# Optimization experiments

Hardware: AMD Instinct MI355X
Metric: run time of the kernel (lower is better)

## Reference

```python
import jax, jax.numpy as jnp
import numpy as np

OUT_H = 7
OUT_W = 7
SPATIAL_SCALE = 0.25
SAMPLING_RATIO = 2  # exact sampling branch (sampling_ratio > 0)
ALIGNED = True


def setup_inputs() -> dict:
    key = jax.random.key(0)
    k1, k2, k3, k4 = jax.random.split(key, 4)
    feat = jax.random.normal(k1, (4, 256, 100, 100), dtype=jnp.float32)
    # rois[K,5]: (batch_idx, x1, y1, x2, y2) in image coords (image ~400px since scale=0.25)
    K = 512
    bidx = jax.random.randint(k2, (K,), 0, 4).astype(jnp.float32)
    xy1 = jax.random.uniform(k3, (K, 2), minval=0.0, maxval=300.0, dtype=jnp.float32)
    wh = jax.random.uniform(k4, (K, 2), minval=20.0, maxval=99.0, dtype=jnp.float32)
    xy2 = xy1 + wh
    rois = jnp.concatenate([bidx[:, None], xy1[:, 0:1], xy1[:, 1:2], xy2[:, 0:1], xy2[:, 1:2]], axis=1)
    return {"input": feat, "rois": rois}


def _roi_align(feat, rois):
    N, C, H, W = feat.shape
    b = rois[:, 0].astype(jnp.int32)  # [K]
    offset = 0.5 if ALIGNED else 0.0
    sw = rois[:, 1] * SPATIAL_SCALE - offset
    sh = rois[:, 2] * SPATIAL_SCALE - offset
    ew = rois[:, 3] * SPATIAL_SCALE - offset
    eh = rois[:, 4] * SPATIAL_SCALE - offset
    rw = ew - sw
    rh = eh - sh
    if not ALIGNED:
        rw = jnp.maximum(rw, 1.0)
        rh = jnp.maximum(rh, 1.0)
    bin_h = rh / OUT_H  # [K]
    bin_w = rw / OUT_W

    ph = jnp.arange(OUT_H, dtype=feat.dtype)
    pw = jnp.arange(OUT_W, dtype=feat.dtype)
    samp = jnp.arange(SAMPLING_RATIO, dtype=feat.dtype) + 0.5  # (i + 0.5)

    # y: [K, OUT_H, SR], x: [K, OUT_W, SR]
    y = sh[:, None, None] + ph[None, :, None] * bin_h[:, None, None] + samp[None, None, :] * (bin_h / SAMPLING_RATIO)[:, None, None]
    x = sw[:, None, None] + pw[None, :, None] * bin_w[:, None, None] + samp[None, None, :] * (bin_w / SAMPLING_RATIO)[:, None, None]

    # bilinear interpolation indices/weights (matches _bilinear_interpolate)
    y = jnp.maximum(y, 0.0)
    x = jnp.maximum(x, 0.0)
    yl = y.astype(jnp.int32)
    xl = x.astype(jnp.int32)
    yh = jnp.where(yl >= H - 1, H - 1, yl + 1)
    yl = jnp.where(yl >= H - 1, H - 1, yl)
    xh = jnp.where(xl >= W - 1, W - 1, xl + 1)
    xl = jnp.where(xl >= W - 1, W - 1, xl)
    ly = y - yl.astype(feat.dtype)
    lx = x - xl.astype(feat.dtype)
    hy = 1.0 - ly
    hx = 1.0 - lx

    def gather(yi, xi):
        # yi: [K,PH,IY], xi: [K,PW,IX] -> [K,PH,IY,PW,IX,C]
        return feat[b[:, None, None, None, None], :,
                    yi[:, :, :, None, None],
                    xi[:, None, None, :, :]]

    v1 = gather(yl, xl)
    v2 = gather(yl, xh)
    v3 = gather(yh, xl)
    v4 = gather(yh, xh)

    out = (jnp.einsum('kpi,kqj,kpiqjc->kcpq', hy, hx, v1)
           + jnp.einsum('kpi,kqj,kpiqjc->kcpq', hy, lx, v2)
           + jnp.einsum('kpi,kqj,kpiqjc->kcpq', ly, hx, v3)
           + jnp.einsum('kpi,kqj,kpiqjc->kcpq', ly, lx, v4))
    count = float(max(SAMPLING_RATIO * SAMPLING_RATIO, 1))
    return out / count  # [K, C, OUT_H, OUT_W]


def reference(input, rois):
    return _roi_align(input, rois)
```

## Files before the change

kernel.cpp:

```cpp
#include <hip/hip_runtime.h>


#define FEAT_C 256
#define FEAT_H 100
#define FEAT_W 100
#define HW     10000
#define NROI   512
#define NBINS  49
#define CPB    8
#define GROUPS 32
#define NPAIR  4
#define YS     14
#define RSTR   60
#define PAIRSTR (YS * RSTR)

typedef float f32x2 __attribute__((ext_vector_type(2)));

__device__ __forceinline__ void samp_geo(float s, float bsz, int idx, int sr_i,
                                         int& lo, float& fr) {
    float v = s + bsz * ((float)idx + ((float)sr_i + 0.5f) * 0.5f);
    v = fmaxf(v, 0.0f);
    int l = (int)v;
    if (l > FEAT_H - 1) l = FEAT_H - 1;
    fr = v - (float)l;
    lo = l;
}

__global__ __launch_bounds__(256, 8) void roialign_fwd(
    const float* __restrict__ feat,
    const float* __restrict__ rois,
    float* __restrict__ out)
{
    __shared__ __align__(16) float s_rows[NPAIR * PAIRSTR];
    __shared__ __align__(16) int2  s_xt[YS];

    const int bid = blockIdx.x;
    const int k   = bid >> 5;
    const int cg  = bid & (GROUPS - 1);
    const int tid = threadIdx.x;

    const float* r = rois + k * 5;
    const int   b  = (int)r[0];
    const float sw = r[1] * 0.25f - 0.5f;
    const float sh = r[2] * 0.25f - 0.5f;
    const float ew = r[3] * 0.25f - 0.5f;
    const float eh = r[4] * 0.25f - 0.5f;
    const float bh = (eh - sh) * (1.0f / 7.0f);
    const float bw = (ew - sw) * (1.0f / 7.0f);

    int x0; float fd;
    samp_geo(sw, bw, 0, 0, x0, fd);
    const int ax0 = x0 & ~3;

    if (tid < YS) {
        int lo; float fr;
        samp_geo(sw, bw, tid >> 1, tid & 1, lo, fr);
        if (lo >= FEAT_W - 1) fr = 0.0f;
        s_xt[tid] = make_int2((lo - ax0) * 2, __float_as_int(fr));
    }

    if (tid < 2 * 98) {
        const int half = tid >= 98;
        const int sid  = tid - 98 * half;
        const int ys   = (sid * 9363) >> 16;
        const int q    = sid - ys * 7;

        int yl; float fry;
        samp_geo(sh, bh, ys >> 1, ys & 1, yl, fry);
        int yh = yl + 1; if (yh > FEAT_H - 1) yh = FEAT_H - 1;
        const float hyw = 1.0f - fry, lyw = fry;

        int col = ax0 + q * 4;
        if (col > FEAT_W - 4) col = FEAT_W - 4;

        const float* fb = feat + (size_t)(b * FEAT_C + cg * CPB) * HW
                        + yl * FEAT_W + col;
        const int dyh = (yh - yl) * FEAT_W;
        float* dbase = s_rows + ys * RSTR + q * 8;

        for (int p = 2 * half; p < 2 * half + 2; p++) {
            const float* c0 = fb + (2 * p) * HW;
            const float* c1 = c0 + HW;
            float4 L0 = *(const float4*)(c0);
            float4 H0 = *(const float4*)(c0 + dyh);
            float4 L1 = *(const float4*)(c1);
            float4 H1 = *(const float4*)(c1 + dyh);
            float4 r0, r1;
            r0.x = L0.x * hyw + H0.x * lyw;  r0.y = L0.y * hyw + H0.y * lyw;
            r0.z = L0.z * hyw + H0.z * lyw;  r0.w = L0.w * hyw + H0.w * lyw;
            r1.x = L1.x * hyw + H1.x * lyw;  r1.y = L1.y * hyw + H1.y * lyw;
            r1.z = L1.z * hyw + H1.z * lyw;  r1.w = L1.w * hyw + H1.w * lyw;
            float* d = dbase + p * PAIRSTR;
            *(float4*)(d)     = make_float4(r0.x, r1.x, r0.y, r1.y);
            *(float4*)(d + 4) = make_float4(r0.z, r1.z, r0.w, r1.w);
        }
    }
    __syncthreads();

    if (tid < 4 * NBINS) {
        const int cp  = (tid * 335) >> 14;
        const int bin = tid - cp * NBINS;
        const int ph  = (bin * 37) >> 8;
        const int pw  = bin - ph * 7;

        const int4 xg = *(const int4*)(&s_xt[2 * pw]);
        const float lx0 = __int_as_float(xg.y), hx0 = 1.0f - lx0;
        const float lx1 = __int_as_float(xg.w), hx1 = 1.0f - lx1;

        const float* P = s_rows + cp * PAIRSTR + (2 * ph) * RSTR;
        f32x2 acc = {0.0f, 0.0f};
        #pragma unroll
        for (int iy = 0; iy < 2; iy++) {
            const float* row = P + iy * RSTR;
            const f32x2* A = (const f32x2*)(row + xg.x);
            f32x2 a0 = A[0], a1 = A[1];
            const f32x2* B = (const f32x2*)(row + xg.z);
            f32x2 b0 = B[0], b1 = B[1];
            acc += a0 * hx0 + a1 * lx0;
            acc += b0 * hx1 + b1 * lx1;
        }
        acc *= 0.25f;

        float* ob = out + ((size_t)k * FEAT_C + cg * CPB + cp * 2) * NBINS + bin;
        ob[0]     = acc.x;
        ob[NBINS] = acc.y;
    }
}

extern "C" void kernel_launch(void* const* d_in, const int* in_sizes, int n_in,
                              void* d_out, int out_size, void* d_ws, size_t ws_size,
                              hipStream_t stream) {
    const float* feat = (const float*)d_in[0];
    const float* rois = (const float*)d_in[1];
    float*       outp = (float*)d_out;
    roialign_fwd<<<dim3(NROI * GROUPS), dim3(256), 0, stream>>>(feat, rois, outp);
}
```

Before: 105.2 us.

## Stage ROI patches via direct global-to-LDS loads with double-buffered channel loop

Each block now handles 32 channels of one ROI instead of 8, iterating over 8 items of 4 channels. A 25x28 feature patch per channel is copied straight into LDS with global_load_lds, double-buffered so the next item's load overlaps the current item's interpolation. The y-interpolation moves from the staging step to the consumer. This cuts block count and the per-block ROI geometry setup, and avoids the register round-trip on loads. The cost is more syncs per block, lower occupancy, and a fixed 25-row patch that must cover the ROI extent.

```diff
diff --git a/kernel.cpp b/kernel.cpp
--- a/kernel.cpp
+++ b/kernel.cpp
@@ -7,14 +7,13 @@
 #define HW     10000
 #define NROI   512
 #define NBINS  49
-#define CPB    8
-#define GROUPS 32
-#define NPAIR  4
-#define YS     14
-#define RSTR   60
-#define PAIRSTR (YS * RSTR)
-
-typedef float f32x2 __attribute__((ext_vector_type(2)));
+#define CPI    4
+#define ITEMS  8
+#define PROWS  25
+#define PSTR   28
+#define CBYTES (PROWS * PSTR * 4)
+#define BUFDW  (CPI * PROWS * PSTR)
+#define BUFBYTES (BUFDW * 4)
 
 __device__ __forceinline__ void samp_geo(float s, float bsz, int idx, int sr_i,
                                          int& lo, float& fr) {
@@ -26,104 +25,109 @@
     lo = l;
 }
 
-__global__ __launch_bounds__(256, 8) void roialign_fwd(
+__global__ __launch_bounds__(256, 7) void roialign_fwd(
     const float* __restrict__ feat,
     const float* __restrict__ rois,
     float* __restrict__ out)
 {
-    __shared__ __align__(16) float s_rows[NPAIR * PAIRSTR];
-    __shared__ __align__(16) int2  s_xt[YS];
+    __shared__ __align__(16) float s_patch[2 * BUFDW];
+    __shared__ __align__(16) int2  s_yt[14];
+    __shared__ __align__(16) int2  s_xt[14];
 
-    const int bid = blockIdx.x;
-    const int k   = bid >> 5;
-    const int cg  = bid & (GROUPS - 1);
-    const int tid = threadIdx.x;
+    const int bid  = blockIdx.x;
+    const int k    = bid >> 3;
+    const int cgrp = bid & 7;
+    const int tid  = threadIdx.x;
 
     const float* r = rois + k * 5;
     const int   b  = (int)r[0];
-    const float sw = r[1] * 0.25f - 0.5f;
-    const float sh = r[2] * 0.25f - 0.5f;
-    const float ew = r[3] * 0.25f - 0.5f;
-    const float eh = r[4] * 0.25f - 0.5f;
+    const float sw = r[1] * 0.25f - 0.5f, sh = r[2] * 0.25f - 0.5f;
+    const float ew = r[3] * 0.25f - 0.5f, eh = r[4] * 0.25f - 0.5f;
     const float bh = (eh - sh) * (1.0f / 7.0f);
     const float bw = (ew - sw) * (1.0f / 7.0f);
 
-    int x0; float fd;
-    samp_geo(sw, bw, 0, 0, x0, fd);
-    const int ax0 = x0 & ~3;
+    int y0, yM, x0, xM; float fd;
+    samp_geo(sh, bh, 0, 0, y0, fd);  samp_geo(sh, bh, 6, 1, yM, fd);
+    samp_geo(sw, bw, 0, 0, x0, fd);  samp_geo(sw, bw, 6, 1, xM, fd);
+    const int ax0  = x0 & ~3;
+    const int rows = yM - y0 + 2;
 
-    if (tid < YS) {
+    if (tid < 14) {
         int lo; float fr;
-        samp_geo(sw, bw, tid >> 1, tid & 1, lo, fr);
+        samp_geo(sh, bh, tid >> 1, tid & 1, lo, fr);
+        s_yt[tid] = make_int2((lo - y0) * (PSTR * 4), __float_as_int(fr));
+    } else if (tid >= 32 && tid < 46) {
+        int t = tid - 32; int lo; float fr;
+        samp_geo(sw, bw, t >> 1, t & 1, lo, fr);
         if (lo >= FEAT_W - 1) fr = 0.0f;
-        s_xt[tid] = make_int2((lo - ax0) * 2, __float_as_int(fr));
+        s_xt[t] = make_int2((lo - ax0) * 4, __float_as_int(fr));
     }
 
-    if (tid < 2 * 98) {
-        const int half = tid >= 98;
-        const int sid  = tid - 98 * half;
-        const int ys   = (sid * 9363) >> 16;
-        const int q    = sid - ys * 7;
+    const int  spy = (tid * 9363) >> 16;
+    const int  sq  = tid - spy * 7;
+    int sy = y0 + spy; if (sy > FEAT_H - 1) sy = FEAT_H - 1;
+    int sc = ax0 + sq * 4; if (sc > FEAT_W - 4) sc = FEAT_W - 4;
+    const int  goff   = sy * FEAT_W + sc;
+    const bool stager = tid < rows * 7;
+    const int  wid    = __builtin_amdgcn_readfirstlane(tid >> 6);
+    const float* fblk = feat + (size_t)(b * FEAT_C + cgrp * 32) * HW;
 
-        int yl; float fry;
-        samp_geo(sh, bh, ys >> 1, ys & 1, yl, fry);
-        int yh = yl + 1; if (yh > FEAT_H - 1) yh = FEAT_H - 1;
-        const float hyw = 1.0f - fry, lyw = fry;
+    auto dma = [&](int item, int selb) {
+        if (stager) {
+            const float* g0 = fblk + (size_t)item * (CPI * HW) + goff;
+            char* l0 = (char*)s_patch + selb * BUFBYTES + wid * 1024;
+            #pragma unroll
+            for (int c = 0; c < CPI; c++)
+                __builtin_amdgcn_global_load_lds(
+                    (const __attribute__((address_space(1))) void*)(g0 + c * HW),
+                    (__attribute__((address_space(3))) void*)(l0 + c * CBYTES),
+                    16, 0, 0);
+        }
+    };
 
-        int col = ax0 + q * 4;
-        if (col > FEAT_W - 4) col = FEAT_W - 4;
-
-        const float* fb = feat + (size_t)(b * FEAT_C + cg * CPB) * HW
-                        + yl * FEAT_W + col;
-        const int dyh = (yh - yl) * FEAT_W;
-        float* dbase = s_rows + ys * RSTR + q * 8;
-
-        for (int p = 2 * half; p < 2 * half + 2; p++) {
-            const float* c0 = fb + (2 * p) * HW;
-            const float* c1 = c0 + HW;
-            float4 L0 = *(const float4*)(c0);
-            float4 H0 = *(const float4*)(c0 + dyh);
-            float4 L1 = *(const float4*)(c1);
-            float4 H1 = *(const float4*)(c1 + dyh);
-            float4 r0, r1;
-            r0.x = L0.x * hyw + H0.x * lyw;  r0.y = L0.y * hyw + H0.y * lyw;
-            r0.z = L0.z * hyw + H0.z * lyw;  r0.w = L0.w * hyw + H0.w * lyw;
-            r1.x = L1.x * hyw + H1.x * lyw;  r1.y = L1.y * hyw + H1.y * lyw;
-            r1.z = L1.z * hyw + H1.z * lyw;  r1.w = L1.w * hyw + H1.w * lyw;
-            float* d = dbase + p * PAIRSTR;
-            *(float4*)(d)     = make_float4(r0.x, r1.x, r0.y, r1.y);
-            *(float4*)(d + 4) = make_float4(r0.z, r1.z, r0.w, r1.w);
-        }
-    }
+    dma(0, 0);
     __syncthreads();
 
-    if (tid < 4 * NBINS) {
-        const int cp  = (tid * 335) >> 14;
-        const int bin = tid - cp * NBINS;
-        const int ph  = (bin * 37) >> 8;
-        const int pw  = bin - ph * 7;
+    const int cch  = (tid * 335) >> 14;
+    const int cbin = tid - cch * 49;
+    const int cph  = (cbin * 37) >> 8;
+    const int cpw  = cbin - cph * 7;
+    const int4 yg = *(const int4*)&s_yt[2 * cph];
+    const int4 xg = *(const int4*)&s_xt[2 * cpw];
+    const float lyA = __int_as_float(yg.y), hyA = 1.0f - lyA;
+    const float lyB = __int_as_float(yg.w), hyB = 1.0f - lyB;
+    const float lx0 = __int_as_float(xg.y), hx0 = 1.0f - lx0;
+    const float lx1 = __int_as_float(xg.w), hx1 = 1.0f - lx1;
+    const int   choff = cch * CBYTES;
+    float* const oblk = out + (size_t)(k * FEAT_C + cgrp * 32) * NBINS;
 
-        const int4 xg = *(const int4*)(&s_xt[2 * pw]);
-        const float lx0 = __int_as_float(xg.y), hx0 = 1.0f - lx0;
-        const float lx1 = __int_as_float(xg.w), hx1 = 1.0f - lx1;
+    int sel = 0;
+    #pragma unroll
+    for (int i = 0; i < ITEMS; i++) {
+        if (i < ITEMS - 1) dma(i + 1, sel ^ 1);
 
-        const float* P = s_rows + cp * PAIRSTR + (2 * ph) * RSTR;
-        f32x2 acc = {0.0f, 0.0f};
-        #pragma unroll
-        for (int iy = 0; iy < 2; iy++) {
-            const float* row = P + iy * RSTR;
-            const f32x2* A = (const f32x2*)(row + xg.x);
-            f32x2 a0 = A[0], a1 = A[1];
-            const f32x2* B = (const f32x2*)(row + xg.z);
-            f32x2 b0 = B[0], b1 = B[1];
-            acc += a0 * hx0 + a1 * lx0;
-            acc += b0 * hx1 + b1 * lx1;
+        if (tid < CPI * NBINS) {
+            const char* cb  = (const char*)s_patch + sel * BUFBYTES + choff;
+            const char* rA  = cb + yg.x;
+            const char* rB  = cb + yg.z;
+            const float* a00 = (const float*)(rA + xg.x);
+            const float* a01 = (const float*)(rA + xg.z);
+            const float* a10 = (const float*)(rA + PSTR * 4 + xg.x);
+            const float* a11 = (const float*)(rA + PSTR * 4 + xg.z);
+            const float* b00 = (const float*)(rB + xg.x);
+            const float* b01 = (const float*)(rB + xg.z);
+            const float* b10 = (const float*)(rB + PSTR * 4 + xg.x);
+            const float* b11 = (const float*)(rB + PSTR * 4 + xg.z);
+            float loA = hx0 * a00[0] + lx0 * a00[1] + hx1 * a01[0] + lx1 * a01[1];
+            float hiA = hx0 * a10[0] + lx0 * a10[1] + hx1 * a11[0] + lx1 * a11[1];
+            float loB = hx0 * b00[0] + lx0 * b00[1] + hx1 * b01[0] + lx1 * b01[1];
+            float hiB = hx0 * b10[0] + lx0 * b10[1] + hx1 * b11[0] + lx1 * b11[1];
+            float acc = hyA * loA + lyA * hiA + hyB * loB + lyB * hiB;
+            oblk[i * (CPI * NBINS) + tid] = acc * 0.25f;
         }
-        acc *= 0.25f;
 
-        float* ob = out + ((size_t)k * FEAT_C + cg * CPB + cp * 2) * NBINS + bin;
-        ob[0]     = acc.x;
-        ob[NBINS] = acc.y;
+        if (i < ITEMS - 1) __syncthreads();
+        sel ^= 1;
     }
 }
 
@@ -133,5 +137,5 @@
     const float* feat = (const float*)d_in[0];
     const float* rois = (const float*)d_in[1];
     float*       outp = (float*)d_out;
-    roialign_fwd<<<dim3(NROI * GROUPS), dim3(256), 0, stream>>>(feat, rois, outp);
+    roialign_fwd<<<dim3(NROI * 8), dim3(256), 0, stream>>>(feat, rois, outp);
 }
```

Measured after the change: 109.4 us. +4.0%, slower.
